# Kernel tuning notes

Hardware: AMD Instinct MI355X
Metric: run time of the kernel (lower is better)

## Reference

```python
import jax, jax.numpy as jnp
import numpy as np

B, Q, D = 4, 8192, 256
L, P = 2, 8
H0 = W0 = 128
H1 = W1 = 64
EPS = 1e-5


def _bilinear_sample(feat, gx, gy):
    """grid_sample bilinear, padding_mode='border', align_corners=False.
    feat: (B, D, H, W); gx, gy: (B, N) in [-1, 1]. Returns (B, N, D)."""
    b, d, h, w = feat.shape
    # unnormalize (align_corners=False)
    x = ((gx + 1.0) * w - 1.0) * 0.5
    y = ((gy + 1.0) * h - 1.0) * 0.5
    # border padding: clamp coords into valid range
    x = jnp.clip(x, 0.0, w - 1.0)
    y = jnp.clip(y, 0.0, h - 1.0)
    x0 = jnp.floor(x)
    y0 = jnp.floor(y)
    wx = x - x0
    wy = y - y0
    x0i = x0.astype(jnp.int32)
    y0i = y0.astype(jnp.int32)
    x1i = jnp.minimum(x0i + 1, w - 1)
    y1i = jnp.minimum(y0i + 1, h - 1)
    fhw = feat.reshape(b, d, h * w)  # (B, D, H*W)

    def gather(iy, ix):
        idx = iy * w + ix  # (B, N)
        return jnp.take_along_axis(fhw, idx[:, None, :], axis=2)  # (B, D, N)

    v00 = gather(y0i, x0i)
    v01 = gather(y0i, x1i)
    v10 = gather(y1i, x0i)
    v11 = gather(y1i, x1i)
    wxb = wx[:, None, :]
    wyb = wy[:, None, :]
    top = v00 * (1.0 - wxb) + v01 * wxb
    bot = v10 * (1.0 - wxb) + v11 * wxb
    out = top * (1.0 - wyb) + bot * wyb  # (B, D, N)
    return out.transpose(0, 2, 1)  # (B, N, D)


def setup_inputs() -> dict:
    key = jax.random.key(0)
    ks = jax.random.split(key, 12)
    s = 0.02
    return {
        "q": jax.random.normal(ks[0], (B, Q, D), jnp.float32),
        "map0": jax.random.normal(ks[1], (B, D, H0, W0), jnp.float32),
        "map1": jax.random.normal(ks[2], (B, D, H1, W1), jnp.float32),
        "base_ref": jax.random.uniform(ks[3], (B, L, 2), jnp.float32),
        "Wrd": jax.random.normal(ks[4], (D, L * 2), jnp.float32) * s,
        "brd": jax.random.normal(ks[5], (L * 2,), jnp.float32) * s,
        "Woff": jax.random.normal(ks[6], (D, L * P * 2), jnp.float32) * s,
        "boff": jax.random.normal(ks[7], (L * P * 2,), jnp.float32) * 1.5,
        "Wattn": jax.random.normal(ks[8], (D, L * P), jnp.float32) * s,
        "battn": jax.random.normal(ks[9], (L * P,), jnp.float32) * s,
        "Wout": jax.random.normal(ks[10], (D, D), jnp.float32) * s,
        "bout": jax.random.normal(ks[11], (D,), jnp.float32) * s,
    }


def reference(q, map0, map1, base_ref, Wrd, brd, Woff, boff, Wattn, battn, Wout, bout):
    b, qn, d = q.shape
    maps = [map0, map1]
    # per-level reference points, refined through inverse-sigmoid space
    base = jnp.clip(base_ref, EPS, 1.0 - EPS)[:, None, :, :]  # (B, 1, L, 2)
    logit_base = jnp.log(base / (1.0 - base))
    ref_delta = (q @ Wrd + brd).reshape(b, qn, L, 2)
    ref = jax.nn.sigmoid(logit_base + ref_delta)  # (B, Q, L, 2)
    offsets = (q @ Woff + boff).reshape(b, qn, L, P, 2)
    attn_logits = (q @ Wattn + battn).reshape(b, qn, L * P)
    attn = jax.nn.softmax(attn_logits, axis=-1).reshape(b, qn, L, P)

    out = jnp.zeros((b, qn, d), jnp.float32)
    for level, feat in enumerate(maps):
        h, w = feat.shape[2], feat.shape[3]
        normalizer = jnp.array([w, h], jnp.float32)
        loc = ref[:, :, level, None, :] + offsets[:, :, level] / normalizer  # (B,Q,P,2)
        if level == 1:
            loc = jnp.stack([loc[..., 0], jnp.remainder(loc[..., 1], 1.0)], axis=-1)
        loc = loc * 2.0 - 1.0
        gx = loc[..., 0].reshape(b, qn * P)
        gy = loc[..., 1].reshape(b, qn * P)
        samp = _bilinear_sample(feat, gx, gy).reshape(b, qn, P, d)
        out = out + jnp.sum(samp * attn[:, :, level, :, None], axis=2)
    return out @ Wout + bout
```

## Files before the change

### kernel.cpp

```cpp
#include <hip/hip_runtime.h>
#include <hip/hip_bf16.h>

#define BQ 4
#define QN 8192
#define DD 256
#define LL 2
#define H0c 128
#define W0c 128
#define H1c 64
#define W1c 64
#define EPSF 1e-5f

typedef unsigned short ushort_t;
typedef __attribute__((ext_vector_type(8))) short short8;
typedef __attribute__((ext_vector_type(8))) unsigned short ushortx8;
typedef __attribute__((ext_vector_type(4))) float floatx4;
typedef __attribute__((ext_vector_type(4))) _Float16 half4;

static __device__ __forceinline__ float lo16f(unsigned int d) {
    union { unsigned int u; float f; } x; x.u = d << 16; return x.f;
}
static __device__ __forceinline__ float hi16f(unsigned int d) {
    union { unsigned int u; float f; } x; x.u = d & 0xFFFF0000u; return x.f;
}
static __device__ __forceinline__ unsigned short f2bf(float f) {
    __hip_bfloat16 h = __float2bfloat16(f);
    return __builtin_bit_cast(unsigned short, h);
}

#define T0B 16384
#define T1B 4096
#define TWB 64
__global__ __launch_bounds__(256) void prep(const float* __restrict__ map0, const float* __restrict__ map1,
                                            const float* __restrict__ Wout,
                                            const float* __restrict__ Wrd, const float* __restrict__ brd,
                                            const float* __restrict__ Woff, const float* __restrict__ boff,
                                            const float* __restrict__ Wattn, const float* __restrict__ battn,
                                            __hip_bfloat16* __restrict__ mapT0, __hip_bfloat16* __restrict__ mapT1,
                                            __hip_bfloat16* __restrict__ WoutT,
                                            float* __restrict__ Wall, float* __restrict__ bias64) {
    __shared__ float tile[32][33];
    int blk = blockIdx.x;
    int tx = threadIdx.x, ty = threadIdx.y;
    const float* in; __hip_bfloat16* outp; int HW, b, c0, hw0;
    if (blk < T0B) {
        int l = blk; b = l / (512 * 8); int r = l % (512 * 8);
        c0 = (r / 512) * 32; hw0 = (r % 512) * 32;
        in = map0; outp = mapT0; HW = H0c * W0c;
    } else if (blk < T0B + T1B) {
        int l = blk - T0B; b = l / (128 * 8); int r = l % (128 * 8);
        c0 = (r / 128) * 32; hw0 = (r % 128) * 32;
        in = map1; outp = mapT1; HW = H1c * W1c;
    } else if (blk < T0B + T1B + TWB) {
        int l = blk - T0B - T1B; b = 0;
        c0 = (l / 8) * 32; hw0 = (l % 8) * 32;
        in = Wout; outp = WoutT; HW = DD;
    } else {
        int l = blk - T0B - T1B - TWB;
        int tid = ty * 32 + tx;
        int idx = l * 256 + tid;
        int k = idx >> 6, c = idx & 63;
        float v = (c < 4)  ? Wrd[k * 4 + c]
                : (c < 36) ? Woff[k * 32 + (c - 4)]
                : (c < 52) ? Wattn[k * 16 + (c - 36)]
                : 0.f;
        Wall[idx] = v;
        if (idx < 64) {
            float bv = (idx < 4)  ? brd[idx]
                     : (idx < 36) ? boff[idx - 4]
                     : (idx < 52) ? battn[idx - 36]
                     : 0.f;
            bias64[idx] = bv;
        }
        return;
    }
    const float* inb = in + (size_t)b * DD * HW;
    __hip_bfloat16* outb = outp + (size_t)b * DD * HW;
#pragma unroll
    for (int j = 0; j < 32; j += 8)
        tile[ty + j][tx] = inb[(size_t)(c0 + ty + j) * HW + hw0 + tx];
    __syncthreads();
#pragma unroll
    for (int j = 0; j < 32; j += 8)
        outb[(size_t)(hw0 + ty + j) * DD + c0 + tx] = __float2bfloat16(tile[tx][ty + j]);
}

__global__ __launch_bounds__(256) void proj_desc(const float* __restrict__ q,
                                                 const float* __restrict__ Wall,
                                                 const float* __restrict__ bias64,
                                                 const float* __restrict__ base_ref,
                                                 int2* __restrict__ dsi,
                                                 half4* __restrict__ dsw) {
    __shared__ float As[32][68];
    __shared__ float Bs[32][64];
    __shared__ float prs[64][68];
    int tid = threadIdx.x;
    int tx = tid & 15, ty = tid >> 4;
    int m0 = blockIdx.x * 64;
    float acc[4][4] = {};

    for (int kt = 0; kt < DD; kt += 32) {
#pragma unroll
        for (int j = 0; j < 8; j++) {
            int e = tid + 256 * j;
            int r = e >> 5, k = e & 31;
            As[k][r] = q[(size_t)(m0 + r) * DD + kt + k];
        }
#pragma unroll
        for (int j = 0; j < 8; j++) {
            int e = tid + 256 * j;
            int k = e >> 6, nn = e & 63;
            Bs[k][nn] = Wall[(size_t)(kt + k) * 64 + nn];
        }
        __syncthreads();
#pragma unroll
        for (int k = 0; k < 32; k++) {
            const float4 a4 = *(const float4*)&As[k][ty * 4];
            const float4 b4 = *(const float4*)&Bs[k][tx * 4];
            acc[0][0] += a4.x * b4.x; acc[0][1] += a4.x * b4.y; acc[0][2] += a4.x * b4.z; acc[0][3] += a4.x * b4.w;
            acc[1][0] += a4.y * b4.x; acc[1][1] += a4.y * b4.y; acc[1][2] += a4.y * b4.z; acc[1][3] += a4.y * b4.w;
            acc[2][0] += a4.z * b4.x; acc[2][1] += a4.z * b4.y; acc[2][2] += a4.z * b4.z; acc[2][3] += a4.z * b4.w;
            acc[3][0] += a4.w * b4.x; acc[3][1] += a4.w * b4.y; acc[3][2] += a4.w * b4.z; acc[3][3] += a4.w * b4.w;
        }
        __syncthreads();
    }

    float4 bias = *(const float4*)&bias64[tx * 4];
#pragma unroll
    for (int i = 0; i < 4; i++) {
        float4 v;
        v.x = acc[i][0] + bias.x;
        v.y = acc[i][1] + bias.y;
        v.z = acc[i][2] + bias.z;
        v.w = acc[i][3] + bias.w;
        *(float4*)&prs[ty * 4 + i][tx * 4] = v;
    }
    __syncthreads();

    int ql = tid >> 2, sq = tid & 3;
    int n = m0 + ql, b = n >> 13;
    const float* p = prs[ql];

    float mx = p[36];
#pragma unroll
    for (int i = 1; i < 16; i++) mx = fmaxf(mx, p[36 + i]);
    float sum = 0.f;
#pragma unroll
    for (int i = 0; i < 16; i++) sum += __expf(p[36 + i] - mx);
    float inv = 1.f / sum;

#pragma unroll
    for (int u = 0; u < 4; u++) {
        int s = sq * 4 + u;
        int l = s >> 3;
        float a = __expf(p[36 + s] - mx) * inv;

        int W = l ? W1c : W0c;
        int H = l ? H1c : H0c;
        float Wf = (float)W, Hf = (float)H;

        float bx = base_ref[(b * LL + l) * 2 + 0];
        float by = base_ref[(b * LL + l) * 2 + 1];
        bx = fminf(fmaxf(bx, EPSF), 1.f - EPSF);
        by = fminf(fmaxf(by, EPSF), 1.f - EPSF);
        float lgx = logf(bx / (1.f - bx));
        float lgy = logf(by / (1.f - by));
        float refx = 1.f / (1.f + __expf(-(lgx + p[l * 2 + 0])));
        float refy = 1.f / (1.f + __expf(-(lgy + p[l * 2 + 1])));

        float locx = refx + p[4 + s * 2 + 0] / Wf;
        float locy = refy + p[4 + s * 2 + 1] / Hf;
        if (l == 1) locy = locy - floorf(locy);

        float gx = locx * 2.f - 1.f;
        float gy = locy * 2.f - 1.f;
        float x = ((gx + 1.f) * Wf - 1.f) * 0.5f;
        float y = ((gy + 1.f) * Hf - 1.f) * 0.5f;
        x = fminf(fmaxf(x, 0.f), Wf - 1.f);
        y = fminf(fmaxf(y, 0.f), Hf - 1.f);
        float x0f = floorf(x), y0f = floorf(y);
        float wx = x - x0f, wy = y - y0f;
        int x0 = (int)x0f, y0 = (int)y0f;
        unsigned int dx = (x0 + 1 <= W - 1) ? DD : 0;
        unsigned int dy = (y0 + 1 <= H - 1) ? (unsigned)(W * DD) : 0;
        int base = ((b * H + y0) * W + x0) * DD;

        float omx = 1.f - wx, omy = 1.f - wy;
        half4 w;
        w[0] = (_Float16)(a * omx * omy);
        w[1] = (_Float16)(a * wx  * omy);
        w[2] = (_Float16)(a * omx * wy);
        w[3] = (_Float16)(a * wx  * wy);

        dsi[(size_t)n * 16 + s] = make_int2(base, (int)((dy << 16) | dx));
        dsw[(size_t)n * 16 + s] = w;
    }
}

__global__ __launch_bounds__(256, 3) void sample_kernel(const ushort_t* __restrict__ mapT0,
                                                        const ushort_t* __restrict__ mapT1,
                                                        const int2* __restrict__ dsi,
                                                        const half4* __restrict__ dsw,
                                                        ushort_t* __restrict__ S) {
    int tid = threadIdx.x;
    int lx = tid & 63;
    int n = blockIdx.x * 8 + (tid >> 6) * 2 + (lx >> 5);
    int c8 = (lx & 31) * 8;
    const int2*  gi = dsi + (size_t)n * 16;
    const half4* gw = dsw + (size_t)n * 16;

    int2 g[16]; half4 wh[16];
#pragma unroll
    for (int s = 0; s < 16; s++) { g[s] = gi[s]; wh[s] = gw[s]; }

    float acc[8];
#pragma unroll
    for (int i = 0; i < 8; i++) acc[i] = 0.f;

#pragma unroll
    for (int grp = 0; grp < 4; grp++) {
        const ushort_t* mp = (grp < 2) ? mapT0 : mapT1;
        uint4 u[4][4];
#pragma unroll
        for (int j = 0; j < 4; j++) {
            int s = grp * 4 + j;
            int dx = g[s].y & 0xffff;
            int dy = (int)(((unsigned int)g[s].y) >> 16);
            const ushort_t* p0 = mp + g[s].x + c8;
            u[j][0] = *(const uint4*)(p0);
            u[j][1] = *(const uint4*)(p0 + dx);
            u[j][2] = *(const uint4*)(p0 + dy);
            u[j][3] = *(const uint4*)(p0 + dx + dy);
        }
#pragma unroll
        for (int j = 0; j < 4; j++) {
            int s = grp * 4 + j;
            float w0 = (float)wh[s][0], w1 = (float)wh[s][1], w2 = (float)wh[s][2], w3 = (float)wh[s][3];
#pragma unroll
            for (int corner = 0; corner < 4; corner++) {
                uint4 v = u[j][corner];
                float wc = (corner == 0) ? w0 : (corner == 1) ? w1 : (corner == 2) ? w2 : w3;
                acc[0] += wc * lo16f(v.x); acc[1] += wc * hi16f(v.x);
                acc[2] += wc * lo16f(v.y); acc[3] += wc * hi16f(v.y);
                acc[4] += wc * lo16f(v.z); acc[5] += wc * hi16f(v.z);
                acc[6] += wc * lo16f(v.w); acc[7] += wc * hi16f(v.w);
            }
        }
    }
    ushortx8 o;
#pragma unroll
    for (int i = 0; i < 8; i++) o[i] = f2bf(acc[i]);
    *(ushortx8*)(S + (size_t)n * DD + c8) = o;
}

__global__ __launch_bounds__(256) void out_mfma(const ushort_t* __restrict__ S,
                                                const ushort_t* __restrict__ WT,
                                                const float* __restrict__ bout,
                                                float* __restrict__ out) {
    __shared__ ushort_t wlds[64][256];
    int tid = threadIdx.x;
    int n0c = blockIdx.x * 64;
    int wave = tid >> 6, lane = tid & 63;
    int m0 = blockIdx.y * 64 + wave * 16;
    int mrow = lane & 15, quad = lane >> 4;

#pragma unroll
    for (int i = 0; i < 8; i++) {
        int idx = tid + 256 * i;
        int row = idx >> 5, c = idx & 31;
        *(uint4*)&wlds[row][(c ^ (row & 31)) * 8] =
            *(const uint4*)(WT + (size_t)(n0c + row) * DD + c * 8);
    }
    __syncthreads();

    const ushort_t* Sp = S + (size_t)(m0 + mrow) * DD + quad * 8;
    short8 a[8];
#pragma unroll
    for (int k = 0; k < 8; k++) a[k] = *(const short8*)(Sp + k * 32);

    floatx4 acc[4];
#pragma unroll
    for (int nt = 0; nt < 4; nt++) acc[nt] = {0.f, 0.f, 0.f, 0.f};

#pragma unroll
    for (int nt = 0; nt < 4; nt++) {
        int row = nt * 16 + mrow;
#pragma unroll
        for (int k = 0; k < 8; k++) {
            int c = k * 4 + quad;
            short8 b = *(const short8*)&wlds[row][(c ^ (row & 31)) * 8];
            acc[nt] = __builtin_amdgcn_mfma_f32_16x16x32_bf16(a[k], b, acc[nt], 0, 0, 0);
        }
    }

    int rbase = quad * 4;
#pragma unroll
    for (int nt = 0; nt < 4; nt++) {
        float bv = bout[n0c + nt * 16 + mrow];
#pragma unroll
        for (int r = 0; r < 4; r++) {
            out[(size_t)(m0 + rbase + r) * DD + n0c + nt * 16 + mrow] = acc[nt][r] + bv;
        }
    }
}

extern "C" void kernel_launch(void* const* d_in, const int* in_sizes, int n_in,
                              void* d_out, int out_size, void* d_ws, size_t ws_size,
                              hipStream_t stream) {
    const float* q        = (const float*)d_in[0];
    const float* map0     = (const float*)d_in[1];
    const float* map1     = (const float*)d_in[2];
    const float* base_ref = (const float*)d_in[3];
    const float* Wrd      = (const float*)d_in[4];
    const float* brd      = (const float*)d_in[5];
    const float* Woff     = (const float*)d_in[6];
    const float* boff     = (const float*)d_in[7];
    const float* Wattn    = (const float*)d_in[8];
    const float* battn    = (const float*)d_in[9];
    const float* Wout     = (const float*)d_in[10];
    const float* bout     = (const float*)d_in[11];
    float* out = (float*)d_out;

    char* ws = (char*)d_ws;
    __hip_bfloat16* mapT0  = (__hip_bfloat16*)(ws + 0);
    __hip_bfloat16* mapT1  = (__hip_bfloat16*)(ws + 33554432);
    __hip_bfloat16* WoutT  = (__hip_bfloat16*)(ws + 41943040);
    float*          Wall   = (float*)(ws + 42074112);
    float*          bias64 = (float*)(ws + 42139648);
    int2*           dsi    = (int2*)(ws + 42139904);
    half4*          dsw    = (half4*)(ws + 46334208);
    ushort_t*       Sbuf   = (ushort_t*)(ws + 50528512);

    prep<<<dim3(T0B + T1B + TWB + 64), dim3(32, 8), 0, stream>>>(
        map0, map1, Wout, Wrd, brd, Woff, boff, Wattn, battn,
        mapT0, mapT1, WoutT, Wall, bias64);

    proj_desc<<<dim3(BQ * QN / 64), dim3(256), 0, stream>>>(q, Wall, bias64, base_ref, dsi, dsw);

    sample_kernel<<<dim3(BQ * QN / 8), dim3(256), 0, stream>>>(
        (const ushort_t*)mapT0, (const ushort_t*)mapT1, dsi, dsw, Sbuf);

    out_mfma<<<dim3(4, BQ * QN / 64), dim3(256), 0, stream>>>(
        Sbuf, (const ushort_t*)WoutT, bout, out);
}
```

Baseline: 246.3 us.

## Transpose only sampled map regions and fuse sampling with output GEMM

The projection kernel now also records, per batch and level, the bounding box of all bilinear corner indices using shared and global atomics. The map transpose moves after projection and skips any 32-wide tile outside that box, so it avoids reading and converting the large feature maps where nothing is sampled. Sampling and the output projection are fused into one kernel that keeps the 16-row sampled tile in LDS and runs MFMA against WoutT read straight from global memory, which removes the intermediate S buffer round trip. The trade-offs are extra atomics, a serial dependency from projection to transpose, and no LDS staging of WoutT in the fused GEMM.

```diff
diff --git a/kernel.cpp b/kernel.cpp
--- a/kernel.cpp
+++ b/kernel.cpp
@@ -11,6 +11,9 @@
 #define W1c 64
 #define EPSF 1e-5f
 
+#define T0B 16384
+#define T1B 4096
+
 typedef unsigned short ushort_t;
 typedef __attribute__((ext_vector_type(8))) short short8;
 typedef __attribute__((ext_vector_type(8))) unsigned short ushortx8;
@@ -28,35 +31,27 @@
     return __builtin_bit_cast(unsigned short, h);
 }
 
-#define T0B 16384
-#define T1B 4096
-#define TWB 64
-__global__ __launch_bounds__(256) void prep(const float* __restrict__ map0, const float* __restrict__ map1,
-                                            const float* __restrict__ Wout,
-                                            const float* __restrict__ Wrd, const float* __restrict__ brd,
-                                            const float* __restrict__ Woff, const float* __restrict__ boff,
-                                            const float* __restrict__ Wattn, const float* __restrict__ battn,
-                                            __hip_bfloat16* __restrict__ mapT0, __hip_bfloat16* __restrict__ mapT1,
-                                            __hip_bfloat16* __restrict__ WoutT,
-                                            float* __restrict__ Wall, float* __restrict__ bias64) {
+__global__ __launch_bounds__(256) void prep_pack(const float* __restrict__ Wout,
+                                                 const float* __restrict__ Wrd, const float* __restrict__ brd,
+                                                 const float* __restrict__ Woff, const float* __restrict__ boff,
+                                                 const float* __restrict__ Wattn, const float* __restrict__ battn,
+                                                 __hip_bfloat16* __restrict__ WoutT,
+                                                 float* __restrict__ Wall, float* __restrict__ bias64,
+                                                 int* __restrict__ bb) {
     __shared__ float tile[32][33];
     int blk = blockIdx.x;
     int tx = threadIdx.x, ty = threadIdx.y;
-    const float* in; __hip_bfloat16* outp; int HW, b, c0, hw0;
-    if (blk < T0B) {
-        int l = blk; b = l / (512 * 8); int r = l % (512 * 8);
-        c0 = (r / 512) * 32; hw0 = (r % 512) * 32;
-        in = map0; outp = mapT0; HW = H0c * W0c;
-    } else if (blk < T0B + T1B) {
-        int l = blk - T0B; b = l / (128 * 8); int r = l % (128 * 8);
-        c0 = (r / 128) * 32; hw0 = (r % 128) * 32;
-        in = map1; outp = mapT1; HW = H1c * W1c;
-    } else if (blk < T0B + T1B + TWB) {
-        int l = blk - T0B - T1B; b = 0;
-        c0 = (l / 8) * 32; hw0 = (l % 8) * 32;
-        in = Wout; outp = WoutT; HW = DD;
+    if (blk < 64) {
+        int c0 = (blk / 8) * 32, hw0 = (blk % 8) * 32;
+#pragma unroll
+        for (int j = 0; j < 32; j += 8)
+            tile[ty + j][tx] = Wout[(size_t)(c0 + ty + j) * DD + hw0 + tx];
+        __syncthreads();
+#pragma unroll
+        for (int j = 0; j < 32; j += 8)
+            WoutT[(size_t)(hw0 + ty + j) * DD + c0 + tx] = __float2bfloat16(tile[tx][ty + j]);
     } else {
-        int l = blk - T0B - T1B - TWB;
+        int l = blk - 64;
         int tid = ty * 32 + tx;
         int idx = l * 256 + tid;
         int k = idx >> 6, c = idx & 63;
@@ -72,17 +67,9 @@
                      : 0.f;
             bias64[idx] = bv;
         }
-        return;
-    }
-    const float* inb = in + (size_t)b * DD * HW;
-    __hip_bfloat16* outb = outp + (size_t)b * DD * HW;
-#pragma unroll
-    for (int j = 0; j < 32; j += 8)
-        tile[ty + j][tx] = inb[(size_t)(c0 + ty + j) * HW + hw0 + tx];
-    __syncthreads();
-#pragma unroll
-    for (int j = 0; j < 32; j += 8)
-        outb[(size_t)(hw0 + ty + j) * DD + c0 + tx] = __float2bfloat16(tile[tx][ty + j]);
+        if (idx < 16)      bb[idx] = 0x7fffffff;
+        else if (idx < 32) bb[idx] = 0;
+    }
 }
 
 __global__ __launch_bounds__(256) void proj_desc(const float* __restrict__ q,
@@ -90,13 +77,17 @@
                                                  const float* __restrict__ bias64,
                                                  const float* __restrict__ base_ref,
                                                  int2* __restrict__ dsi,
-                                                 half4* __restrict__ dsw) {
+                                                 half4* __restrict__ dsw,
+                                                 int* __restrict__ bb) {
     __shared__ float As[32][68];
     __shared__ float Bs[32][64];
     __shared__ float prs[64][68];
+    __shared__ int lbb[8];
     int tid = threadIdx.x;
     int tx = tid & 15, ty = tid >> 4;
     int m0 = blockIdx.x * 64;
+    if (tid < 4) lbb[tid] = 0x7fffffff;
+    else if (tid < 8) lbb[tid] = 0;
     float acc[4][4] = {};
 
     for (int kt = 0; kt < DD; kt += 32) {
@@ -139,6 +130,7 @@
 
     int ql = tid >> 2, sq = tid & 3;
     int n = m0 + ql, b = n >> 13;
+    int lvl = sq >> 1;
     const float* p = prs[ql];
 
     float mx = p[36];
@@ -148,6 +140,8 @@
 #pragma unroll
     for (int i = 0; i < 16; i++) sum += __expf(p[36 + i] - mx);
     float inv = 1.f / sum;
+
+    int mnx = 0x7fffffff, mny = 0x7fffffff, mxx = 0, mxy = 0;
 
 #pragma unroll
     for (int u = 0; u < 4; u++) {
@@ -185,6 +179,9 @@
         unsigned int dy = (y0 + 1 <= H - 1) ? (unsigned)(W * DD) : 0;
         int base = ((b * H + y0) * W + x0) * DD;
 
+        mnx = min(mnx, x0); mny = min(mny, y0);
+        mxx = max(mxx, x0 + (dx ? 1 : 0)); mxy = max(mxy, y0 + (dy ? 1 : 0));
+
         float omx = 1.f - wx, omy = 1.f - wy;
         half4 w;
         w[0] = (_Float16)(a * omx * omy);
@@ -195,111 +192,131 @@
         dsi[(size_t)n * 16 + s] = make_int2(base, (int)((dy << 16) | dx));
         dsw[(size_t)n * 16 + s] = w;
     }
-}
-
-__global__ __launch_bounds__(256, 3) void sample_kernel(const ushort_t* __restrict__ mapT0,
-                                                        const ushort_t* __restrict__ mapT1,
-                                                        const int2* __restrict__ dsi,
-                                                        const half4* __restrict__ dsw,
-                                                        ushort_t* __restrict__ S) {
+
+    atomicMin(&lbb[lvl * 2 + 0], mnx);
+    atomicMin(&lbb[lvl * 2 + 1], mny);
+    atomicMax(&lbb[4 + lvl * 2 + 0], mxx);
+    atomicMax(&lbb[4 + lvl * 2 + 1], mxy);
+    __syncthreads();
+    if (tid < 4)      atomicMin(&bb[(b * 2 + (tid >> 1)) * 2 + (tid & 1)], lbb[tid]);
+    else if (tid < 8) atomicMax(&bb[16 + (b * 2 + ((tid - 4) >> 1)) * 2 + ((tid - 4) & 1)], lbb[tid]);
+}
+
+__global__ __launch_bounds__(256) void map_transpose(const float* __restrict__ map0, const float* __restrict__ map1,
+                                                     __hip_bfloat16* __restrict__ mapT0, __hip_bfloat16* __restrict__ mapT1,
+                                                     const int* __restrict__ bb) {
+    __shared__ float tile[32][33];
+    int blk = blockIdx.x;
+    int tx = threadIdx.x, ty = threadIdx.y;
+    const float* in; __hip_bfloat16* outp; int HW, b, c0, hw0, l, W;
+    if (blk < T0B) {
+        l = 0; b = blk / (512 * 8); int r = blk % (512 * 8);
+        c0 = (r / 512) * 32; hw0 = (r % 512) * 32;
+        in = map0; outp = mapT0; HW = H0c * W0c; W = W0c;
+    } else {
+        l = 1; int t = blk - T0B; b = t / (128 * 8); int r = t % (128 * 8);
+        c0 = (r / 128) * 32; hw0 = (r % 128) * 32;
+        in = map1; outp = mapT1; HW = H1c * W1c; W = W1c;
+    }
+    int y = hw0 / W, xt = hw0 % W;
+    int bbi = (b * 2 + l) * 2;
+    int mnx = bb[bbi], mny = bb[bbi + 1], mxx = bb[16 + bbi], mxy = bb[16 + bbi + 1];
+    if (y < mny || y > mxy || xt > mxx || xt + 31 < mnx) return;
+
+    const float* inb = in + (size_t)b * DD * HW;
+    __hip_bfloat16* outb = outp + (size_t)b * DD * HW;
+#pragma unroll
+    for (int j = 0; j < 32; j += 8)
+        tile[ty + j][tx] = inb[(size_t)(c0 + ty + j) * HW + hw0 + tx];
+    __syncthreads();
+#pragma unroll
+    for (int j = 0; j < 32; j += 8)
+        outb[(size_t)(hw0 + ty + j) * DD + c0 + tx] = __float2bfloat16(tile[tx][ty + j]);
+}
+
+__global__ __launch_bounds__(256, 4) void sample_out(const ushort_t* __restrict__ mapT0,
+                                                     const ushort_t* __restrict__ mapT1,
+                                                     const int2* __restrict__ dsi,
+                                                     const half4* __restrict__ dsw,
+                                                     const ushort_t* __restrict__ WT,
+                                                     const float* __restrict__ bout,
+                                                     float* __restrict__ out) {
+    __shared__ ushort_t S[16][264];
     int tid = threadIdx.x;
-    int lx = tid & 63;
-    int n = blockIdx.x * 8 + (tid >> 6) * 2 + (lx >> 5);
-    int c8 = (lx & 31) * 8;
-    const int2*  gi = dsi + (size_t)n * 16;
-    const half4* gw = dsw + (size_t)n * 16;
-
-    int2 g[16]; half4 wh[16];
-#pragma unroll
-    for (int s = 0; s < 16; s++) { g[s] = gi[s]; wh[s] = gw[s]; }
-
-    float acc[8];
-#pragma unroll
-    for (int i = 0; i < 8; i++) acc[i] = 0.f;
-
-#pragma unroll
-    for (int grp = 0; grp < 4; grp++) {
-        const ushort_t* mp = (grp < 2) ? mapT0 : mapT1;
-        uint4 u[4][4];
-#pragma unroll
-        for (int j = 0; j < 4; j++) {
-            int s = grp * 4 + j;
-            int dx = g[s].y & 0xffff;
-            int dy = (int)(((unsigned int)g[s].y) >> 16);
-            const ushort_t* p0 = mp + g[s].x + c8;
-            u[j][0] = *(const uint4*)(p0);
-            u[j][1] = *(const uint4*)(p0 + dx);
-            u[j][2] = *(const uint4*)(p0 + dy);
-            u[j][3] = *(const uint4*)(p0 + dx + dy);
-        }
-#pragma unroll
-        for (int j = 0; j < 4; j++) {
-            int s = grp * 4 + j;
-            float w0 = (float)wh[s][0], w1 = (float)wh[s][1], w2 = (float)wh[s][2], w3 = (float)wh[s][3];
-#pragma unroll
-            for (int corner = 0; corner < 4; corner++) {
-                uint4 v = u[j][corner];
-                float wc = (corner == 0) ? w0 : (corner == 1) ? w1 : (corner == 2) ? w2 : w3;
-                acc[0] += wc * lo16f(v.x); acc[1] += wc * hi16f(v.x);
-                acc[2] += wc * lo16f(v.y); acc[3] += wc * hi16f(v.y);
-                acc[4] += wc * lo16f(v.z); acc[5] += wc * hi16f(v.z);
-                acc[6] += wc * lo16f(v.w); acc[7] += wc * hi16f(v.w);
+    int wave = tid >> 6, lane = tid & 63;
+    int m0 = blockIdx.x * 16;
+    int halfq = lane >> 5;
+    int c8 = (lane & 31) * 8;
+
+#pragma unroll
+    for (int iter = 0; iter < 2; iter++) {
+        int nl = wave * 4 + iter * 2 + halfq;
+        int n = m0 + nl;
+        const int2*  gi = dsi + (size_t)n * 16;
+        const half4* gw = dsw + (size_t)n * 16;
+        int2 g[16]; half4 wh[16];
+#pragma unroll
+        for (int s = 0; s < 16; s++) { g[s] = gi[s]; wh[s] = gw[s]; }
+
+        float acc[8];
+#pragma unroll
+        for (int i = 0; i < 8; i++) acc[i] = 0.f;
+
+#pragma unroll
+        for (int grp = 0; grp < 4; grp++) {
+            const ushort_t* mp = (grp < 2) ? mapT0 : mapT1;
+            uint4 u[4][4];
+#pragma unroll
+            for (int j = 0; j < 4; j++) {
+                int s = grp * 4 + j;
+                int dx = g[s].y & 0xffff;
+                int dy = (int)(((unsigned int)g[s].y) >> 16);
+                const ushort_t* p0 = mp + g[s].x + c8;
+                u[j][0] = *(const uint4*)(p0);
+                u[j][1] = *(const uint4*)(p0 + dx);
+                u[j][2] = *(const uint4*)(p0 + dy);
+                u[j][3] = *(const uint4*)(p0 + dx + dy);
             }
-        }
-    }
-    ushortx8 o;
-#pragma unroll
-    for (int i = 0; i < 8; i++) o[i] = f2bf(acc[i]);
-    *(ushortx8*)(S + (size_t)n * DD + c8) = o;
-}
-
-__global__ __launch_bounds__(256) void out_mfma(const ushort_t* __restrict__ S,
-                                                const ushort_t* __restrict__ WT,
-                                                const float* __restrict__ bout,
-                                                float* __restrict__ out) {
-    __shared__ ushort_t wlds[64][256];
-    int tid = threadIdx.x;
-    int n0c = blockIdx.x * 64;
-    int wave = tid >> 6, lane = tid & 63;
-    int m0 = blockIdx.y * 64 + wave * 16;
-    int mrow = lane & 15, quad = lane >> 4;
-
-#pragma unroll
-    for (int i = 0; i < 8; i++) {
-        int idx = tid + 256 * i;
-        int row = idx >> 5, c = idx & 31;
-        *(uint4*)&wlds[row][(c ^ (row & 31)) * 8] =
-            *(const uint4*)(WT + (size_t)(n0c + row) * DD + c * 8);
+#pragma unroll
+            for (int j = 0; j < 4; j++) {
+                int s = grp * 4 + j;
+                float w0 = (float)wh[s][0], w1 = (float)wh[s][1], w2 = (float)wh[s][2], w3 = (float)wh[s][3];
+#pragma unroll
+                for (int corner = 0; corner < 4; corner++) {
+                    uint4 v = u[j][corner];
+                    float wc = (corner == 0) ? w0 : (corner == 1) ? w1 : (corner == 2) ? w2 : w3;
+                    acc[0] += wc * lo16f(v.x); acc[1] += wc * hi16f(v.x);
+                    acc[2] += wc * lo16f(v.y); acc[3] += wc * hi16f(v.y);
+                    acc[4] += wc * lo16f(v.z); acc[5] += wc * hi16f(v.z);
+                    acc[6] += wc * lo16f(v.w); acc[7] += wc * hi16f(v.w);
+                }
+            }
+        }
+        ushortx8 o;
+#pragma unroll
+        for (int i = 0; i < 8; i++) o[i] = f2bf(acc[i]);
+        *(ushortx8*)&S[nl][c8] = o;
     }
     __syncthreads();
 
-    const ushort_t* Sp = S + (size_t)(m0 + mrow) * DD + quad * 8;
+    int row = lane & 15, quad = lane >> 4;
     short8 a[8];
 #pragma unroll
-    for (int k = 0; k < 8; k++) a[k] = *(const short8*)(Sp + k * 32);
-
-    floatx4 acc[4];
-#pragma unroll
-    for (int nt = 0; nt < 4; nt++) acc[nt] = {0.f, 0.f, 0.f, 0.f};
-
-#pragma unroll
-    for (int nt = 0; nt < 4; nt++) {
-        int row = nt * 16 + mrow;
+    for (int k = 0; k < 8; k++) a[k] = *(const short8*)&S[row][quad * 8 + k * 32];
+
+#pragma unroll
+    for (int j = 0; j < 4; j++) {
+        int nt = wave * 4 + j;
+        floatx4 acc4 = {0.f, 0.f, 0.f, 0.f};
 #pragma unroll
         for (int k = 0; k < 8; k++) {
-            int c = k * 4 + quad;
-            short8 b = *(const short8*)&wlds[row][(c ^ (row & 31)) * 8];
-            acc[nt] = __builtin_amdgcn_mfma_f32_16x16x32_bf16(a[k], b, acc[nt], 0, 0, 0);
-        }
-    }
-
-    int rbase = quad * 4;
-#pragma unroll
-    for (int nt = 0; nt < 4; nt++) {
-        float bv = bout[n0c + nt * 16 + mrow];
+            short8 bfr = *(const short8*)(WT + (size_t)(nt * 16 + row) * DD + k * 32 + quad * 8);
+            acc4 = __builtin_amdgcn_mfma_f32_16x16x32_bf16(a[k], bfr, acc4, 0, 0, 0);
+        }
+        float bv = bout[nt * 16 + row];
 #pragma unroll
         for (int r = 0; r < 4; r++) {
-            out[(size_t)(m0 + rbase + r) * DD + n0c + nt * 16 + mrow] = acc[nt][r] + bv;
+            out[(size_t)(m0 + quad * 4 + r) * DD + nt * 16 + row] = acc4[r] + bv;
         }
     }
 }
@@ -329,17 +346,16 @@
     float*          bias64 = (float*)(ws + 42139648);
     int2*           dsi    = (int2*)(ws + 42139904);
     half4*          dsw    = (half4*)(ws + 46334208);
-    ushort_t*       Sbuf   = (ushort_t*)(ws + 50528512);
-
-    prep<<<dim3(T0B + T1B + TWB + 64), dim3(32, 8), 0, stream>>>(
-        map0, map1, Wout, Wrd, brd, Woff, boff, Wattn, battn,
-        mapT0, mapT1, WoutT, Wall, bias64);
-
-    proj_desc<<<dim3(BQ * QN / 64), dim3(256), 0, stream>>>(q, Wall, bias64, base_ref, dsi, dsw);
-
-    sample_kernel<<<dim3(BQ * QN / 8), dim3(256), 0, stream>>>(
-        (const ushort_t*)mapT0, (const ushort_t*)mapT1, dsi, dsw, Sbuf);
-
-    out_mfma<<<dim3(4, BQ * QN / 64), dim3(256), 0, stream>>>(
-        Sbuf, (const ushort_t*)WoutT, bout, out);
-}
+    int*            bb     = (int*)(ws + 50528512);
+
+    prep_pack<<<dim3(128), dim3(32, 8), 0, stream>>>(
+        Wout, Wrd, brd, Woff, boff, Wattn, battn, WoutT, Wall, bias64, bb);
+
+    proj_desc<<<dim3(BQ * QN / 64), dim3(256), 0, stream>>>(q, Wall, bias64, base_ref, dsi, dsw, bb);
+
+    map_transpose<<<dim3(T0B + T1B), dim3(32, 8), 0, stream>>>(map0, map1, mapT0, mapT1, bb);
+
+    sample_out<<<dim3(BQ * QN / 16), dim3(256), 0, stream>>>(
+        (const ushort_t*)mapT0, (const ushort_t*)mapT1, dsi, dsw,
+        (const ushort_t*)WoutT, bout, out);
+}
```

Result: slower. 343.3 us (+39.4%).
